# Optimization experiments

Measured on AMD Instinct MI355X. Metric: run time of the kernel, lower is better.

Reference implementation:

```python
import jax, jax.numpy as jnp
import numpy as np

B, S, D = 8, 2048, 128
NEG = -1e9

def setup_inputs() -> dict:
    key = jax.random.key(0)
    kq, kk, kv = jax.random.split(key, 3)
    query = jax.random.normal(kq, (B, S, D), dtype=jnp.float32)
    k_ = jax.random.normal(kk, (B, S, D), dtype=jnp.float32)
    value = jax.random.normal(kv, (B, S, D), dtype=jnp.float32)
    mask = jnp.tril(jnp.ones((S, S), dtype=jnp.int32))  # causal (seq_len, seq_len)
    return {"query": query, "key": k_, "value": value, "mask": mask}

def reference(query, key, value, mask):
    d_k = query.shape[-1]
    # scores: [B, S, S]
    scores = jnp.einsum('bqd,bkd->bqk', query, key) / jnp.sqrt(jnp.asarray(d_k, jnp.float32))
    scores = jnp.where(mask == 0, jnp.asarray(NEG, scores.dtype), scores)
    p_attn = jax.nn.softmax(scores, axis=-1)
    # dropout p=0.0 -> identity
    return jnp.einsum('bqk,bkd->bqd', p_attn, value)
```

## Files before the change

### kernel.cpp

```cpp
#include <hip/hip_runtime.h>


#define BATCH 8
#define SEQ   2048
#define DIM   128
#define CK    256

typedef _Float16 v4h __attribute__((ext_vector_type(4)));
typedef _Float16 v8h __attribute__((ext_vector_type(8)));
typedef float    v4f __attribute__((ext_vector_type(4)));

#define QF_H 0u
#define KF_H 2097152u
#define VF_H 4194304u
#define OP_H 6291456u
#define ML_B 31457280u
#define WS_NEED 31752192u

__constant__ const float kScale = 0.08838834764831845f;
__constant__ const float kScaleL2 = 0.12751743062f;

__global__ __launch_bounds__(256) void prepass(
    const float* __restrict__ K, const float* __restrict__ V,
    _Float16* __restrict__ wsh)
{
    const int b = blockIdx.x;
    const int t = threadIdx.x;
    if (b < 1024) {
        __shared__ float tile[16][132];
        const int batch = b >> 7, vt = b & 127;
        const float* src = V + ((size_t)batch * SEQ + vt * 16) * DIM;
        const int row = t >> 4, col = (t & 15) * 8;
        *(v4f*)&tile[row][col]     = *(const v4f*)(src + (size_t)row * DIM + col);
        *(v4f*)&tile[row][col + 4] = *(const v4f*)(src + (size_t)row * DIM + col + 4);
        __syncthreads();
        const int n = t >> 4, p = (t >> 2) & 3, qd = t & 3;
        v8h h;
        #pragma unroll
        for (int j = 0; j < 8; ++j) {
            const int d  = 32 * p + 16 * (j >> 2) + n;
            const int kk = qd * 4 + (j & 3);
            h[j] = (_Float16)tile[kk][d];
        }
        const int w = n * 64 + ((p * 16 + qd * 4) ^ ((n & 7) << 2));
        *(v8h*)(wsh + VF_H + (size_t)batch * 262144 + vt * 2048 + w * 2) = h;
    } else {
        const int i = (b - 1024) * 256 + t;
        const int seg = i & 15, row = i >> 4;
        const float* src = K + (size_t)row * DIM + seg * 8;
        v4f a = *(const v4f*)src;
        v4f c = *(const v4f*)(src + 4);
        v8h h;
        #pragma unroll
        for (int j = 0; j < 4; ++j) {
            h[j]     = (_Float16)a[j];
            h[j + 4] = (_Float16)c[j];
        }
        const int w = (seg * 4) ^ ((row & 7) << 2);
        *(v8h*)(wsh + KF_H + (size_t)row * DIM + w * 2) = h;
    }
}

__device__ __forceinline__ void dma16(const _Float16* g, const _Float16* l) {
    __builtin_amdgcn_global_load_lds(
        (const __attribute__((address_space(1))) unsigned int*)g,
        (__attribute__((address_space(3))) unsigned int*)(unsigned int)(uintptr_t)l,
        16, 0, 0);
}

__global__ __launch_bounds__(256, 4) void attn_chunk(
    const float* __restrict__ Q, const _Float16* __restrict__ wsh,
    float* __restrict__ Ml, _Float16* __restrict__ Op,
    float* __restrict__ Out)
{
    __shared__ __align__(16) _Float16 lds[16384];

    const int batch = blockIdx.x & 7;
    int g = blockIdx.x >> 3;
    int c = 0;
    for (; c < 8; ++c) { const int cnt = 32 - 4 * c; if (g < cnt) break; g -= cnt; }
    const int wave = threadIdx.x >> 6;
    const int qt = 16 * c + g * 4 + wave;
    const int q0 = qt * 16;
    const int kbeg = c * CK;

    const int lane = threadIdx.x & 63;
    const int n = lane & 15, quad = lane >> 4;
    const size_t bo = (size_t)batch * SEQ * DIM;

    const _Float16* Kf = wsh + KF_H + bo;
    const _Float16* Vf = wsh + VF_H + bo;

    v8h qa[4];
    {
        const float* qp = Q + bo + (size_t)(q0 + n) * DIM + quad * 8;
        #pragma unroll
        for (int p = 0; p < 4; ++p) {
            v4f a = *(const v4f*)(qp + p * 32);
            v4f b2 = *(const v4f*)(qp + p * 32 + 4);
            v8h h;
            #pragma unroll
            for (int j = 0; j < 4; ++j) {
                h[j]     = (_Float16)(a[j] * kScaleL2);
                h[j + 4] = (_Float16)(b2[j] * kScaleL2);
            }
            qa[p] = h;
        }
    }

    const _Float16* gseg = ((wave < 2) ? (Kf + (size_t)kbeg * DIM)
                                       : (Vf + (size_t)(kbeg >> 4) * 2048))
                           + (wave & 1) * 2048;
    const int ldsseg = (wave >> 1) * 4096 + (wave & 1) * 2048;

    int koff[4];
    #pragma unroll
    for (int p = 0; p < 4; ++p)
        koff[p] = n * 128 + (((quad * 4 + p * 16) ^ ((n & 7) << 2)) << 1);

    float l_run = 0.0f;
    v4f of[8];
    #pragma unroll
    for (int dc = 0; dc < 8; ++dc) of[dc] = (v4f){0.f, 0.f, 0.f, 0.f};

    const int qn0 = q0 + n - kbeg;
    const int kq = quad * 4;

    #pragma unroll
    for (int i = 0; i < 4; ++i)
        dma16(gseg + i * 512 + lane * 8, &lds[ldsseg + i * 512]);

    #pragma unroll
    for (int kb = 0; kb < 8; ++kb) {
        __syncthreads();
        if (kb < 7) {
            const _Float16* gs = gseg + (kb + 1) * 4096;
            const int lb = ((kb + 1) & 1) * 8192 + ldsseg;
            #pragma unroll
            for (int i = 0; i < 4; ++i)
                dma16(gs + i * 512 + lane * 8, &lds[lb + i * 512]);
        }
        const int base = (kb & 1) * 8192;
        #pragma unroll
        for (int t16 = 0; t16 < 2; ++t16) {
            v4f s = (v4f){0.f, 0.f, 0.f, 0.f};
            __builtin_amdgcn_s_setprio(1);
            #pragma unroll
            for (int p = 0; p < 4; ++p) {
                v8h kf = *(const v8h*)&lds[base + t16 * 2048 + koff[p]];
                s = __builtin_amdgcn_mfma_f32_16x16x32_f16(kf, qa[p], s, 0, 0, 0);
            }
            __builtin_amdgcn_s_setprio(0);
            v8h vva[4];
            #pragma unroll
            for (int p = 0; p < 4; ++p)
                vva[p] = *(const v8h*)&lds[base + 4096 + t16 * 2048 + koff[p]];
            v4h pf;
            float ps = 0.f;
            #pragma unroll
            for (int r = 0; r < 4; ++r) {
                const float sv = (kb * 32 + t16 * 16 + kq + r > qn0) ? -1e30f : s[r];
                const float p = exp2f(sv);
                ps += p;
                pf[r] = (_Float16)p;
            }
            l_run += ps;
            __builtin_amdgcn_s_setprio(1);
            #pragma unroll
            for (int p = 0; p < 4; ++p) {
                v4h vlo = __builtin_shufflevector(vva[p], vva[p], 0, 1, 2, 3);
                v4h vhi = __builtin_shufflevector(vva[p], vva[p], 4, 5, 6, 7);
                of[2 * p]     = __builtin_amdgcn_mfma_f32_16x16x16f16(vlo, pf, of[2 * p], 0, 0, 0);
                of[2 * p + 1] = __builtin_amdgcn_mfma_f32_16x16x16f16(vhi, pf, of[2 * p + 1], 0, 0, 0);
            }
            __builtin_amdgcn_s_setprio(0);
        }
    }

    l_run += __shfl_xor(l_run, 16);
    l_run += __shfl_xor(l_run, 32);

    if (c == 0 && g < 4) {
        const float rl = 1.0f / l_run;
        float* op = Out + bo + (size_t)(q0 + n) * DIM + quad * 4;
        #pragma unroll
        for (int dc = 0; dc < 8; ++dc)
            *(v4f*)(op + dc * 16) = of[dc] * rl;
        return;
    }

    const int rs = (2048 * c - 128 * c * (c - 1)) * 8
                 + batch * (2048 - CK * c) + (q0 + n - CK * c);
    _Float16* op = Op + (size_t)rs * DIM;
    #pragma unroll
    for (int dc = 0; dc < 8; ++dc) {
        v4h o;
        #pragma unroll
        for (int r = 0; r < 4; ++r) o[r] = (_Float16)of[dc][r];
        *(v4h*)(op + dc * 16 + quad * 4) = o;
    }
    if (quad == 0) Ml[rs] = l_run;
}

__global__ __launch_bounds__(256) void combine(
    const _Float16* __restrict__ Op, const float* __restrict__ Ml,
    float* __restrict__ O)
{
    const int gid = blockIdx.x * 256 + threadIdx.x;
    const size_t e = (size_t)gid * 8;
    const int d = (int)(e & 127);
    const int q = (int)((e >> 7) & 2047);
    const int b = (int)(e >> 18);
    if (q < 256) return;
    const int nc = (q >> 8) + 1;
    float L = 0.f;
    float acc[8] = {0.f, 0.f, 0.f, 0.f, 0.f, 0.f, 0.f, 0.f};
    for (int c = 0; c < nc; ++c) {
        const int rs = (2048 * c - 128 * c * (c - 1)) * 8 + b * (2048 - 256 * c) + (q - 256 * c);
        L += Ml[rs];
        v8h o = *(const v8h*)(Op + (size_t)rs * DIM + d);
        #pragma unroll
        for (int r = 0; r < 8; ++r) acc[r] += (float)o[r];
    }
    const float rl = 1.0f / L;
    v4f o0, o1;
    #pragma unroll
    for (int r = 0; r < 4; ++r) { o0[r] = acc[r] * rl; o1[r] = acc[r + 4] * rl; }
    *(v4f*)(O + e)     = o0;
    *(v4f*)(O + e + 4) = o1;
}

__global__ __launch_bounds__(128) void attn_fwd(
    const float* __restrict__ Q, const float* __restrict__ K,
    const float* __restrict__ V, float* __restrict__ O)
{
    const int batch = blockIdx.x & 7;
    const int qb    = blockIdx.x >> 3;
    const int tid   = threadIdx.x;
    const int wave  = tid >> 6;
    const int lane  = tid & 63;
    const int n     = lane & 15;
    const int quad  = lane >> 4;

    const int q0      = qb * 32 + wave * 16;
    const int my_last = qb * 2 + wave;
    const int nt      = qb * 2 + 2;

    const size_t bo = (size_t)batch * SEQ * DIM;

    __shared__ __align__(16) _Float16 Ks[16 * 136];
    __shared__ __align__(16) _Float16 Vt[128 * 20];
    typedef _Float16 v2h __attribute__((ext_vector_type(2)));

    v4h qf[8];
    {
        const float* qp = Q + bo + (size_t)(q0 + n) * DIM + quad * 4;
        #pragma unroll
        for (int dc = 0; dc < 8; ++dc) {
            v4f qv = *(const v4f*)(qp + dc * 16);
            v4h h;
            #pragma unroll
            for (int i = 0; i < 4; ++i) h[i] = (_Float16)(qv[i] * kScale);
            qf[dc] = h;
        }
    }

    float m_run = -1e30f, l_run = 0.0f;
    v4f of[8];
    #pragma unroll
    for (int dc = 0; dc < 8; ++dc) of[dc] = (v4f){0.f, 0.f, 0.f, 0.f};

    const int krow = tid >> 3;
    const int kcol = (tid & 7) * 16;
    const int vr   = (tid >> 4) * 2;
    const int vc   = (tid & 15) * 4;

    for (int tk = 0; tk < nt; ++tk) {
        const int k0 = tk * 16;
        {
            const float* kp = K + bo + (size_t)(k0 + krow) * DIM + kcol;
            v4f k0v = *(const v4f*)(kp);
            v4f k1v = *(const v4f*)(kp + 4);
            v4f k2v = *(const v4f*)(kp + 8);
            v4f k3v = *(const v4f*)(kp + 12);
            const float* vp = V + bo + (size_t)(k0 + vr) * DIM + vc;
            v4f va0 = *(const v4f*)(vp);
            v4f va1 = *(const v4f*)(vp + DIM);
            v4f vb0 = *(const v4f*)(vp + 64);
            v4f vb1 = *(const v4f*)(vp + DIM + 64);

            v8h h0, h1;
            #pragma unroll
            for (int i = 0; i < 4; ++i) {
                h0[i]     = (_Float16)k0v[i];
                h0[i + 4] = (_Float16)k1v[i];
                h1[i]     = (_Float16)k2v[i];
                h1[i + 4] = (_Float16)k3v[i];
            }
            *(v8h*)&Ks[krow * 136 + kcol]     = h0;
            *(v8h*)&Ks[krow * 136 + kcol + 8] = h1;

            #pragma unroll
            for (int i = 0; i < 4; ++i) {
                v2h p0 = { (_Float16)va0[i], (_Float16)va1[i] };
                v2h p1 = { (_Float16)vb0[i], (_Float16)vb1[i] };
                *(v2h*)&Vt[(vc + i) * 20 + vr]      = p0;
                *(v2h*)&Vt[(vc + 64 + i) * 20 + vr] = p1;
            }
        }
        __syncthreads();

        if (tk <= my_last) {
            v4f s = (v4f){0.f, 0.f, 0.f, 0.f};
            #pragma unroll
            for (int dc = 0; dc < 8; ++dc) {
                v4h kf = *(const v4h*)&Ks[n * 136 + dc * 16 + quad * 4];
                s = __builtin_amdgcn_mfma_f32_16x16x16f16(kf, qf[dc], s, 0, 0, 0);
            }
            if (tk == my_last) {
                #pragma unroll
                for (int r = 0; r < 4; ++r)
                    if (quad * 4 + r > n) s[r] = -1e30f;
            }
            float tm = fmaxf(fmaxf(s[0], s[1]), fmaxf(s[2], s[3]));
            tm = fmaxf(tm, __shfl_xor(tm, 16));
            tm = fmaxf(tm, __shfl_xor(tm, 32));
            const float m_new = fmaxf(m_run, tm);
            const float alpha = __expf(m_run - m_new);
            v4f p;
            #pragma unroll
            for (int r = 0; r < 4; ++r) p[r] = __expf(s[r] - m_new);
            float ps = p[0] + p[1] + p[2] + p[3];
            ps += __shfl_xor(ps, 16);
            ps += __shfl_xor(ps, 32);
            l_run = l_run * alpha + ps;
            m_run = m_new;

            v4h pf;
            #pragma unroll
            for (int r = 0; r < 4; ++r) pf[r] = (_Float16)p[r];

            #pragma unroll
            for (int dc = 0; dc < 8; ++dc) {
                v4h vf = *(const v4h*)&Vt[(dc * 16 + n) * 20 + quad * 4];
                of[dc] *= alpha;
                of[dc] = __builtin_amdgcn_mfma_f32_16x16x16f16(vf, pf, of[dc], 0, 0, 0);
            }
        }
        __syncthreads();
    }

    const float rl = 1.0f / l_run;
    float* op = O + bo + (size_t)(q0 + n) * DIM + quad * 4;
    #pragma unroll
    for (int dc = 0; dc < 8; ++dc) {
        v4f o = of[dc] * rl;
        *(v4f*)(op + dc * 16) = o;
    }
}

extern "C" void kernel_launch(void* const* d_in, const int* in_sizes, int n_in,
                              void* d_out, int out_size, void* d_ws, size_t ws_size,
                              hipStream_t stream) {
    const float* Q = (const float*)d_in[0];
    const float* K = (const float*)d_in[1];
    const float* V = (const float*)d_in[2];
    float* Out = (float*)d_out;

    if (ws_size >= (size_t)WS_NEED) {
        _Float16* wsh = (_Float16*)d_ws;
        _Float16* Op  = wsh + OP_H;
        float*    Ml  = (float*)((char*)d_ws + ML_B);
        prepass<<<dim3(2048), dim3(256), 0, stream>>>(K, V, wsh);
        attn_chunk<<<dim3(8 * 144), dim3(256), 0, stream>>>(Q, wsh, Ml, Op, Out);
        combine<<<dim3(1024), dim3(256), 0, stream>>>(Op, Ml, Out);
    } else {
        attn_fwd<<<dim3(BATCH * (SEQ / 32)), dim3(128), 0, stream>>>(Q, K, V, Out);
    }
}
```

Measured before the change: 112.4 us.

## Drop LDS staging; load K/V fragments directly from global and skip masked tiles

Removes the LDS double-buffer, the global_load_lds DMA and the per-step block barriers, so each wave reads its K and V fragments straight from global memory, which no longer needs the XOR swizzle. The loop now runs only over the unmasked 16-key tiles of its chunk plus one diagonal tile with a precomputed mask, so fully masked tiles are skipped and masking is dropped from the full tiles. The cost is that the four waves no longer share K/V through LDS, so global and L2 traffic rises, and exposed global-load latency may stall the MFMA pipeline.

```diff
diff --git a/kernel.cpp b/kernel.cpp
--- a/kernel.cpp
+++ b/kernel.cpp
@@ -42,7 +42,7 @@
             const int kk = qd * 4 + (j & 3);
             h[j] = (_Float16)tile[kk][d];
         }
-        const int w = n * 64 + ((p * 16 + qd * 4) ^ ((n & 7) << 2));
+        const int w = n * 64 + (p * 16 + qd * 4);
         *(v8h*)(wsh + VF_H + (size_t)batch * 262144 + vt * 2048 + w * 2) = h;
     } else {
         const int i = (b - 1024) * 256 + t;
@@ -56,16 +56,8 @@
             h[j]     = (_Float16)a[j];
             h[j + 4] = (_Float16)c[j];
         }
-        const int w = (seg * 4) ^ ((row & 7) << 2);
-        *(v8h*)(wsh + KF_H + (size_t)row * DIM + w * 2) = h;
-    }
-}
-
-__device__ __forceinline__ void dma16(const _Float16* g, const _Float16* l) {
-    __builtin_amdgcn_global_load_lds(
-        (const __attribute__((address_space(1))) unsigned int*)g,
-        (__attribute__((address_space(3))) unsigned int*)(unsigned int)(uintptr_t)l,
-        16, 0, 0);
+        *(v8h*)(wsh + KF_H + (size_t)row * DIM + seg * 8) = h;
+    }
 }
 
 __global__ __launch_bounds__(256, 4) void attn_chunk(
@@ -73,8 +65,6 @@
     float* __restrict__ Ml, _Float16* __restrict__ Op,
     float* __restrict__ Out)
 {
-    __shared__ __align__(16) _Float16 lds[16384];
-
     const int batch = blockIdx.x & 7;
     int g = blockIdx.x >> 3;
     int c = 0;
@@ -88,8 +78,8 @@
     const int n = lane & 15, quad = lane >> 4;
     const size_t bo = (size_t)batch * SEQ * DIM;
 
-    const _Float16* Kf = wsh + KF_H + bo;
-    const _Float16* Vf = wsh + VF_H + bo;
+    const _Float16* Kt = wsh + KF_H + bo + (size_t)kbeg * DIM;
+    const _Float16* Vt = wsh + VF_H + bo + (size_t)(kbeg >> 4) * 2048;
 
     v8h qa[4];
     {
@@ -108,72 +98,87 @@
         }
     }
 
-    const _Float16* gseg = ((wave < 2) ? (Kf + (size_t)kbeg * DIM)
-                                       : (Vf + (size_t)(kbeg >> 4) * 2048))
-                           + (wave & 1) * 2048;
-    const int ldsseg = (wave >> 1) * 4096 + (wave & 1) * 2048;
-
     int koff[4];
     #pragma unroll
     for (int p = 0; p < 4; ++p)
-        koff[p] = n * 128 + (((quad * 4 + p * 16) ^ ((n & 7) << 2)) << 1);
+        koff[p] = n * 128 + (quad * 4 + p * 16) * 2;
 
     float l_run = 0.0f;
     v4f of[8];
     #pragma unroll
     for (int dc = 0; dc < 8; ++dc) of[dc] = (v4f){0.f, 0.f, 0.f, 0.f};
 
-    const int qn0 = q0 + n - kbeg;
+    const int Gp = 4 * g + wave;
+    const int nfull = (Gp < 16) ? Gp : 16;
     const int kq = quad * 4;
-
-    #pragma unroll
-    for (int i = 0; i < 4; ++i)
-        dma16(gseg + i * 512 + lane * 8, &lds[ldsseg + i * 512]);
-
-    #pragma unroll
-    for (int kb = 0; kb < 8; ++kb) {
-        __syncthreads();
-        if (kb < 7) {
-            const _Float16* gs = gseg + (kb + 1) * 4096;
-            const int lb = ((kb + 1) & 1) * 8192 + ldsseg;
-            #pragma unroll
-            for (int i = 0; i < 4; ++i)
-                dma16(gs + i * 512 + lane * 8, &lds[lb + i * 512]);
-        }
-        const int base = (kb & 1) * 8192;
-        #pragma unroll
-        for (int t16 = 0; t16 < 2; ++t16) {
-            v4f s = (v4f){0.f, 0.f, 0.f, 0.f};
-            __builtin_amdgcn_s_setprio(1);
-            #pragma unroll
-            for (int p = 0; p < 4; ++p) {
-                v8h kf = *(const v8h*)&lds[base + t16 * 2048 + koff[p]];
-                s = __builtin_amdgcn_mfma_f32_16x16x32_f16(kf, qa[p], s, 0, 0, 0);
-            }
-            __builtin_amdgcn_s_setprio(0);
-            v8h vva[4];
-            #pragma unroll
-            for (int p = 0; p < 4; ++p)
-                vva[p] = *(const v8h*)&lds[base + 4096 + t16 * 2048 + koff[p]];
-            v4h pf;
-            float ps = 0.f;
-            #pragma unroll
-            for (int r = 0; r < 4; ++r) {
-                const float sv = (kb * 32 + t16 * 16 + kq + r > qn0) ? -1e30f : s[r];
-                const float p = exp2f(sv);
-                ps += p;
-                pf[r] = (_Float16)p;
-            }
-            l_run += ps;
-            __builtin_amdgcn_s_setprio(1);
-            #pragma unroll
-            for (int p = 0; p < 4; ++p) {
-                v4h vlo = __builtin_shufflevector(vva[p], vva[p], 0, 1, 2, 3);
-                v4h vhi = __builtin_shufflevector(vva[p], vva[p], 4, 5, 6, 7);
-                of[2 * p]     = __builtin_amdgcn_mfma_f32_16x16x16f16(vlo, pf, of[2 * p], 0, 0, 0);
-                of[2 * p + 1] = __builtin_amdgcn_mfma_f32_16x16x16f16(vhi, pf, of[2 * p + 1], 0, 0, 0);
-            }
-            __builtin_amdgcn_s_setprio(0);
+    bool dmask[4];
+    #pragma unroll
+    for (int r = 0; r < 4; ++r) dmask[r] = (kq + r > n);
+
+    for (int tt = 0; tt < nfull; ++tt) {
+        const _Float16* kp = Kt + (size_t)tt * 2048;
+        const _Float16* vp = Vt + (size_t)tt * 2048;
+        v4f s = (v4f){0.f, 0.f, 0.f, 0.f};
+        __builtin_amdgcn_s_setprio(1);
+        #pragma unroll
+        for (int p = 0; p < 4; ++p) {
+            v8h kf = *(const v8h*)(kp + koff[p]);
+            s = __builtin_amdgcn_mfma_f32_16x16x32_f16(kf, qa[p], s, 0, 0, 0);
+        }
+        __builtin_amdgcn_s_setprio(0);
+        v8h vva[4];
+        #pragma unroll
+        for (int p = 0; p < 4; ++p)
+            vva[p] = *(const v8h*)(vp + koff[p]);
+        v4h pf;
+        float ps = 0.f;
+        #pragma unroll
+        for (int r = 0; r < 4; ++r) {
+            const float p = exp2f(s[r]);
+            ps += p;
+            pf[r] = (_Float16)p;
+        }
+        l_run += ps;
+        __builtin_amdgcn_s_setprio(1);
+        #pragma unroll
+        for (int p = 0; p < 4; ++p) {
+            v4h vlo = __builtin_shufflevector(vva[p], vva[p], 0, 1, 2, 3);
+            v4h vhi = __builtin_shufflevector(vva[p], vva[p], 4, 5, 6, 7);
+            of[2 * p]     = __builtin_amdgcn_mfma_f32_16x16x16f16(vlo, pf, of[2 * p], 0, 0, 0);
+            of[2 * p + 1] = __builtin_amdgcn_mfma_f32_16x16x16f16(vhi, pf, of[2 * p + 1], 0, 0, 0);
+        }
+        __builtin_amdgcn_s_setprio(0);
+    }
+
+    if (Gp < 16) {
+        const _Float16* kp = Kt + (size_t)Gp * 2048;
+        const _Float16* vp = Vt + (size_t)Gp * 2048;
+        v4f s = (v4f){0.f, 0.f, 0.f, 0.f};
+        #pragma unroll
+        for (int p = 0; p < 4; ++p) {
+            v8h kf = *(const v8h*)(kp + koff[p]);
+            s = __builtin_amdgcn_mfma_f32_16x16x32_f16(kf, qa[p], s, 0, 0, 0);
+        }
+        v8h vva[4];
+        #pragma unroll
+        for (int p = 0; p < 4; ++p)
+            vva[p] = *(const v8h*)(vp + koff[p]);
+        v4h pf;
+        float ps = 0.f;
+        #pragma unroll
+        for (int r = 0; r < 4; ++r) {
+            const float sv = dmask[r] ? -1e30f : s[r];
+            const float p = exp2f(sv);
+            ps += p;
+            pf[r] = (_Float16)p;
+        }
+        l_run += ps;
+        #pragma unroll
+        for (int p = 0; p < 4; ++p) {
+            v4h vlo = __builtin_shufflevector(vva[p], vva[p], 0, 1, 2, 3);
+            v4h vhi = __builtin_shufflevector(vva[p], vva[p], 4, 5, 6, 7);
+            of[2 * p]     = __builtin_amdgcn_mfma_f32_16x16x16f16(vlo, pf, of[2 * p], 0, 0, 0);
+            of[2 * p + 1] = __builtin_amdgcn_mfma_f32_16x16x16f16(vhi, pf, of[2 * p + 1], 0, 0, 0);
         }
     }
 
```

New measurement: 166.6 us. 48.3% more time.
